# Optimization experiments

Measured on AMD Instinct MI355X. Metric: run time of the kernel, lower is better.

## Reference

```python
import jax, jax.numpy as jnp
import numpy as np

NUM_HEADS = 8
NS = 27  # 3x3x3 deformable samples per query


def _resize1d(x, axis, new):
    # linear resize along one axis, align_corners=False (matches F.interpolate); identity if size matches
    old = x.shape[axis]
    if old == new:
        return x
    pos = (jnp.arange(new, dtype=jnp.float32) + 0.5) * (old / new) - 0.5
    f = jnp.floor(pos)
    w = pos - f
    i0 = jnp.clip(f, 0, old - 1).astype(jnp.int32)
    i1 = jnp.clip(f + 1, 0, old - 1).astype(jnp.int32)
    shp = [1] * x.ndim
    shp[axis] = new
    w = w.reshape(shp)
    return jnp.take(x, i0, axis=axis) * (1 - w) + jnp.take(x, i1, axis=axis) * w


def _rel_to_abs(x):
    # x: (b, d, h, w, w+NS-1) -> (b, d, h, w, NS) via the pad/reshape shifting trick
    b, d, h, w, c = x.shape
    x = jnp.pad(x, ((0, 0), (0, 0), (0, 0), (0, 0), (0, 1)))
    x = x.reshape(b, d, h, w * (c + 1))
    x = jnp.pad(x, ((0, 0), (0, 0), (0, 0), (0, NS - 1)))
    x = x.reshape(b, d, h, w + 1, NS + w - 1)
    return x[:, :, :, :w, w - 1:]


def _rel_logits_1d(q, rel_k):
    # q: (BH, 1, A, B, C, hd); rel_k: (C+NS-1, hd) -> (BH, A, B, C, NS)
    logits = jnp.einsum('nzxywd,rd->nzxywr', q, rel_k)
    n, z, a, b, c, r = logits.shape
    return _rel_to_abs(logits.reshape(n, z * a, b, c, r))


def _pos_emb(q, rel_depth, rel_height, rel_width, D, H, W):
    # q: (BH, 1, D, H, W, hd) -> (BH, D, H, W, NS)
    rw = _resize1d(rel_width, 0, W + NS - 1)
    rh = _resize1d(rel_height, 0, H + NS - 1)
    rd = _resize1d(rel_depth, 0, D + NS - 1)
    lw = _rel_logits_1d(q, rw)            # (BH, D, H, W, NS)
    qh = jnp.swapaxes(q, 3, 4)            # (BH, 1, D, W, H, hd)
    lh = _rel_logits_1d(qh, rh)           # (BH, D, W, H, NS)
    qd = jnp.swapaxes(qh, 2, 4)           # (BH, 1, H, W, D, hd)
    ld = _rel_logits_1d(qd, rd)           # (BH, H, W, D, NS)
    # trilinear resize of lh/ld to (D, H, W) over spatial axes (identity when D==H==W)
    for ax, tgt in ((1, D), (2, H), (3, W)):
        lh = _resize1d(lh, ax, tgt)
        ld = _resize1d(ld, ax, tgt)
    return lw + lh + ld


def _deform_unfold3d(x, offset):
    # x: (BH, C, D, H, W); offset: (BH, NS*3, D, H, W) -> (BH, C*NS, D*H*W)
    BH, C, D, H, W = x.shape
    off = offset.reshape(BH, NS, 3, D, H, W)
    k = jnp.arange(NS)
    kz = (k // 9 - 1).astype(jnp.float32)
    ky = (k // 3 % 3 - 1).astype(jnp.float32)
    kx = (k % 3 - 1).astype(jnp.float32)
    zz, yy, xx = jnp.meshgrid(jnp.arange(D, dtype=jnp.float32),
                              jnp.arange(H, dtype=jnp.float32),
                              jnp.arange(W, dtype=jnp.float32), indexing='ij')
    pz = zz + kz[:, None, None, None] + off[:, :, 0]   # (BH, NS, D, H, W)
    py = yy + ky[:, None, None, None] + off[:, :, 1]
    px = xx + kx[:, None, None, None] + off[:, :, 2]
    z0 = jnp.floor(pz); y0 = jnp.floor(py); x0 = jnp.floor(px)
    wz = pz - z0; wy = py - y0; wx = px - x0
    z0 = z0.astype(jnp.int32); y0 = y0.astype(jnp.int32); x0 = x0.astype(jnp.int32)
    S = D * H * W
    xf = x.reshape(BH, C, S)
    acc = jnp.zeros((BH, C, NS * S), dtype=x.dtype)
    for dz in (0, 1):
        for dy in (0, 1):
            for dx in (0, 1):
                zi = z0 + dz; yi = y0 + dy; xi = x0 + dx
                valid = ((zi >= 0) & (zi < D) & (yi >= 0) & (yi < H) & (xi >= 0) & (xi < W)).astype(x.dtype)
                w = (wz if dz else 1 - wz) * (wy if dy else 1 - wy) * (wx if dx else 1 - wx) * valid
                idx = (jnp.clip(zi, 0, D - 1) * H + jnp.clip(yi, 0, H - 1)) * W + jnp.clip(xi, 0, W - 1)
                g = jnp.take_along_axis(xf, idx.reshape(BH, 1, NS * S), axis=2)  # (BH, C, NS*S)
                acc = acc + g * w.reshape(BH, 1, NS * S)
    return acc.reshape(BH, C * NS, S)


def _forward(x, w_qkv, w_proj, b_proj, w_off, rel_depth, rel_height, rel_width, D, H, W):
    B, N, C = x.shape
    nh = NUM_HEADS
    hd = C // nh
    scale = hd ** -0.5
    BH = B * nh
    qkv = (x @ w_qkv.T).reshape(B, N, 3, nh, hd)
    q = qkv[:, :, 0].transpose(0, 2, 1, 3)  # (B, nh, N, hd)
    k = qkv[:, :, 1].transpose(0, 2, 1, 3)
    v = qkv[:, :, 2].transpose(0, 2, 1, 3)
    offset = (x.reshape(B, N, nh, hd) @ w_off.T).transpose(0, 2, 3, 1).reshape(BH, NS * 3, D, H, W)
    kmap = k.transpose(0, 1, 3, 2).reshape(BH, hd, D, H, W)
    vmap = v.transpose(0, 1, 3, 2).reshape(BH, hd, D, H, W)
    ks = _deform_unfold3d(kmap, offset).transpose(0, 2, 1).reshape(B, nh, N, hd, NS)
    vs = _deform_unfold3d(vmap, offset).reshape(B, nh, hd, NS, N).transpose(0, 1, 4, 3, 2)  # (B, nh, N, NS, hd)
    attn = jnp.einsum('bhnd,bhnds->bhns', q, ks) * scale
    pos = _pos_emb(q.reshape(BH, 1, D, H, W, hd), rel_depth, rel_height, rel_width, D, H, W).reshape(B, nh, N, NS)
    attn = jax.nn.softmax(attn + pos, axis=-1)
    out = jnp.einsum('bhns,bhnsd->bhnd', attn, vs).transpose(0, 2, 1, 3).reshape(B, N, C)
    return out @ w_proj.T + b_proj


def setup_inputs():
    key = jax.random.key(0)
    ks = jax.random.split(key, 8)
    B, D, H, W, C = 1, 16, 16, 16, 512
    N = D * H * W
    hd = C // NUM_HEADS
    return {
        'x': jax.random.normal(ks[0], (B, N, C), dtype=jnp.float32),
        'w_qkv': jax.random.normal(ks[1], (3 * C, C), dtype=jnp.float32) * 0.02,
        'w_proj': jax.random.normal(ks[2], (C, C), dtype=jnp.float32) * 0.02,
        'b_proj': jnp.zeros((C,), dtype=jnp.float32),
        'w_off': jax.random.normal(ks[3], (NS * 3, hd), dtype=jnp.float32) * 0.01,
        'rel_depth': jax.random.normal(ks[4], (D + NS - 1, hd), dtype=jnp.float32) * hd ** -0.5,
        'rel_height': jax.random.normal(ks[5], (H + NS - 1, hd), dtype=jnp.float32) * hd ** -0.5,
        'rel_width': jax.random.normal(ks[6], (W + NS - 1, hd), dtype=jnp.float32) * hd ** -0.5,
        'D': D, 'H': H, 'W': W,
    }


def reference(x, w_qkv, w_proj, b_proj, w_off, rel_depth, rel_height, rel_width, D, H, W):
    return _forward(x, w_qkv, w_proj, b_proj, w_off, rel_depth, rel_height, rel_width, D, H, W)
```

## Files before the change

### kernel.cpp

```cpp
#include <hip/hip_runtime.h>
#include <hip/hip_fp16.h>
#include <math.h>
#include <stdint.h>

#define NH    8
#define HD    64
#define NTOK  4096
#define CDIM  512
#define NSAMP 27

typedef __attribute__((ext_vector_type(8))) _Float16 half8;
typedef __attribute__((ext_vector_type(4))) float floatx4;
typedef unsigned short ushort_t;

__device__ __forceinline__ ushort_t f16b(float f) {
  return __half_as_ushort(__float2half(f));
}
__device__ __forceinline__ __half2 u2h2(uint32_t u) { return __builtin_bit_cast(__half2, u); }
__device__ __forceinline__ uint32_t h22u(__half2 h) { return __builtin_bit_cast(uint32_t, h); }

__device__ __forceinline__ float wave_sum_lane63(float x) {
#define DPP_STEP(ctrl, rmask)                                                   \
  { int t = __builtin_amdgcn_update_dpp(0, __float_as_int(x), ctrl, rmask, 0xf, \
                                        true);                                  \
    x += __int_as_float(t); }
  DPP_STEP(0x111, 0xf)
  DPP_STEP(0x112, 0xf)
  DPP_STEP(0x114, 0xf)
  DPP_STEP(0x118, 0xf)
  DPP_STEP(0x142, 0xa)
  DPP_STEP(0x143, 0xc)
#undef DPP_STEP
  return x;
}

__global__ __launch_bounds__(256) void k_cvt(const float* __restrict__ x,
                                             const float* __restrict__ wq,
                                             const float* __restrict__ wp,
                                             const float* __restrict__ w_off,
                                             const float* __restrict__ rel_d,
                                             const float* __restrict__ rel_h,
                                             const float* __restrict__ rel_w,
                                             ushort_t* __restrict__ xb,
                                             ushort_t* __restrict__ wqb,
                                             ushort_t* __restrict__ wpb,
                                             ushort_t* __restrict__ w_offh,
                                             ushort_t* __restrict__ relh) {
  int i = blockIdx.x * 256 + threadIdx.x;
  const float4* src = nullptr;
  ushort_t* dst;
  int off;
  float4 v = make_float4(0.f, 0.f, 0.f, 0.f);
  if (i < 524288)      { src = (const float4*)x;  dst = xb;  off = i; }
  else if (i < 720896) { src = (const float4*)wq; dst = wqb; off = i - 524288; }
  else if (i < 786432) { src = (const float4*)wp; dst = wpb; off = i - 720896; }
  else {
    int t = i - 786432;
    if (t < 2048) {
      off = t;
      int e = t * 4, row = e >> 6;
      if (row < 81) v = *(const float4*)&w_off[e];
      dst = w_offh;
    } else {
      off = t - 2048;
      int e = off * 4, row = e >> 6, col = e & 63;
      if (row < 42)       v = *(const float4*)&rel_w[row * 64 + col];
      else if (row < 84)  v = *(const float4*)&rel_h[(row - 42) * 64 + col];
      else if (row < 126) v = *(const float4*)&rel_d[(row - 84) * 64 + col];
      dst = relh;
    }
  }
  if (src) v = src[off];
  ushort4 o = make_ushort4(f16b(v.x), f16b(v.y), f16b(v.z), f16b(v.w));
  *(ushort4*)&dst[(size_t)off * 4] = o;
}

__global__ __launch_bounds__(256) void k_qkv(const ushort_t* __restrict__ Ah,
                                             const ushort_t* __restrict__ Bth,
                                             ushort_t* __restrict__ qh16,
                                             uint32_t* __restrict__ kvb) {
  __shared__ __align__(16) ushort_t As[128 * 32];
  __shared__ __align__(16) ushort_t Bs[128 * 32];
  const int tid = threadIdx.x;
  const int wave = tid >> 6, lane = tid & 63;
  const int wr = wave >> 1, wc = wave & 1;
  const int m15 = lane & 15, quad = lane >> 4;
  const int bm = blockIdx.x, bn = blockIdx.y;
  floatx4 acc[4][4];
#pragma unroll
  for (int i = 0; i < 4; i++)
#pragma unroll
    for (int j = 0; j < 4; j++) acc[i][j] = {0.f, 0.f, 0.f, 0.f};

  const int r0 = tid >> 2, c0 = (tid & 3) * 8;
  const int r1 = r0 + 64;
  for (int k0 = 0; k0 < 512; k0 += 32) {
    *(uint4*)&As[r0 * 32 + c0] = *(const uint4*)&Ah[(size_t)(bm * 128 + r0) * 512 + k0 + c0];
    *(uint4*)&As[r1 * 32 + c0] = *(const uint4*)&Ah[(size_t)(bm * 128 + r1) * 512 + k0 + c0];
    *(uint4*)&Bs[r0 * 32 + c0] = *(const uint4*)&Bth[(size_t)(bn * 128 + r0) * 512 + k0 + c0];
    *(uint4*)&Bs[r1 * 32 + c0] = *(const uint4*)&Bth[(size_t)(bn * 128 + r1) * 512 + k0 + c0];
    __syncthreads();
    half8 af[4], bf[4];
#pragma unroll
    for (int i = 0; i < 4; i++)
      af[i] = *(const half8*)&As[(wr * 64 + i * 16 + m15) * 32 + quad * 8];
#pragma unroll
    for (int j = 0; j < 4; j++)
      bf[j] = *(const half8*)&Bs[(wc * 64 + j * 16 + m15) * 32 + quad * 8];
#pragma unroll
    for (int i = 0; i < 4; i++)
#pragma unroll
      for (int j = 0; j < 4; j++)
        acc[i][j] = __builtin_amdgcn_mfma_f32_16x16x32_f16(af[i], bf[j], acc[i][j], 0, 0, 0);
    __syncthreads();
  }

  ushort_t* kvh16 = (ushort_t*)kvb;
#pragma unroll
  for (int i = 0; i < 4; i++)
#pragma unroll
    for (int j = 0; j < 4; j++) {
      int col = bn * 128 + wc * 64 + j * 16 + m15;
      int t = col >> 9;
      int h = (col >> 6) & 7;
      int d = col & 63;
#pragma unroll
      for (int r = 0; r < 4; r++) {
        int row = bm * 128 + wr * 64 + i * 16 + quad * 4 + r;
        size_t idx = ((size_t)h * NTOK + row) * 64 + d;
        float v = acc[i][j][r];
        if (t == 0) qh16[idx] = f16b(v);
        else kvh16[idx * 2 + (t - 1)] = f16b(v);
      }
    }
}

__global__ __launch_bounds__(256) void k_aux(const ushort_t* __restrict__ xh,
                                             const ushort_t* __restrict__ qh16,
                                             const ushort_t* __restrict__ w_offh,
                                             const ushort_t* __restrict__ relh,
                                             float* __restrict__ ob,
                                             float* __restrict__ Pb) {
  __shared__ __align__(16) ushort_t As[128 * 32];
  __shared__ __align__(16) ushort_t Bs[128 * 32];
  const int tid = threadIdx.x;
  const int wave = tid >> 6, lane = tid & 63;
  const int wr = wave >> 1, wc = wave & 1;
  const int m15 = lane & 15, quad = lane >> 4;
  const int bm = blockIdx.x;
  const int mode = blockIdx.y >> 3, h = blockIdx.y & 7;

  const ushort_t* A;  int lda;
  const ushort_t* B;
  float* C;  int NC;
  if (mode == 0) { A = xh + h * 64;                  lda = 512; B = w_offh; C = ob + (size_t)h * NTOK * 81;  NC = 81; }
  else           { A = qh16 + (size_t)h * NTOK * 64; lda = 64;  B = relh;   C = Pb + (size_t)h * NTOK * 126; NC = 126; }

  floatx4 acc[4][4];
#pragma unroll
  for (int i = 0; i < 4; i++)
#pragma unroll
    for (int j = 0; j < 4; j++) acc[i][j] = {0.f, 0.f, 0.f, 0.f};

  const int r0 = tid >> 2, c0 = (tid & 3) * 8;
  const int r1 = r0 + 64;
  for (int k0 = 0; k0 < 64; k0 += 32) {
    *(uint4*)&As[r0 * 32 + c0] = *(const uint4*)&A[(size_t)(bm * 128 + r0) * lda + k0 + c0];
    *(uint4*)&As[r1 * 32 + c0] = *(const uint4*)&A[(size_t)(bm * 128 + r1) * lda + k0 + c0];
    *(uint4*)&Bs[r0 * 32 + c0] = *(const uint4*)&B[(size_t)r0 * 64 + k0 + c0];
    *(uint4*)&Bs[r1 * 32 + c0] = *(const uint4*)&B[(size_t)r1 * 64 + k0 + c0];
    __syncthreads();
    half8 af[4], bf[4];
#pragma unroll
    for (int i = 0; i < 4; i++)
      af[i] = *(const half8*)&As[(wr * 64 + i * 16 + m15) * 32 + quad * 8];
#pragma unroll
    for (int j = 0; j < 4; j++)
      bf[j] = *(const half8*)&Bs[(wc * 64 + j * 16 + m15) * 32 + quad * 8];
#pragma unroll
    for (int i = 0; i < 4; i++)
#pragma unroll
      for (int j = 0; j < 4; j++)
        acc[i][j] = __builtin_amdgcn_mfma_f32_16x16x32_f16(af[i], bf[j], acc[i][j], 0, 0, 0);
    __syncthreads();
  }

#pragma unroll
  for (int i = 0; i < 4; i++)
#pragma unroll
    for (int j = 0; j < 4; j++) {
      int col = wc * 64 + j * 16 + m15;
      if (col < NC) {
#pragma unroll
        for (int r = 0; r < 4; r++) {
          int row = bm * 128 + wr * 64 + i * 16 + quad * 4 + r;
          C[(size_t)row * NC + col] = acc[i][j][r];
        }
      }
    }
}

__global__ __launch_bounds__(256) void k_attn(const ushort_t* __restrict__ qh16,
                                              const uint32_t* __restrict__ kvb,
                                              const float* __restrict__ obuf,
                                              const float* __restrict__ Pbuf,
                                              ushort_t* __restrict__ attb16) {
  __shared__ int      s_off[4][NSAMP][8];
  __shared__ uint32_t s_cwh[4][NSAMP][8];
  __shared__ uint32_t vpair[4][14][64];
  __shared__ float    s_dots[4][NSAMP];
  __shared__ uint32_t s_wp[4][14];
  const int bid = blockIdx.x;
  const int h = bid & 7;
  const int wave = threadIdx.x >> 6;
  const int lane = threadIdx.x & 63;
  const int n = (bid >> 3) * 4 + wave;
  const int z = n >> 8, y = (n >> 4) & 15, xq = n & 15;
  const float qd = __half2float(__ushort_as_half(qh16[((size_t)h * NTOK + n) * 64 + lane]));
  const char* kvc = (const char*)(kvb + (size_t)h * NTOK * 64);
  const uint32_t lane4 = (uint32_t)lane * 4u;

  if (lane < 54) {
    const int s = lane >> 1, half = lane & 1;
    const float* op = &obuf[((size_t)h * NTOK + n) * 81 + s * 3];
    float oz = op[0], oy = op[1], ox = op[2];
    float pz = (float)(z + (s / 9) - 1) + oz;
    float py = (float)(y + ((s / 3) % 3) - 1) + oy;
    float px = (float)(xq + (s % 3) - 1) + ox;
    float fz = floorf(pz), fy = floorf(py), fx = floorf(px);
    float wz = pz - fz, wy = py - fy, wx = px - fx;
    int z0 = (int)fz, y0 = (int)fy, x0 = (int)fx;
    int      oarr[4];
    uint32_t warr[4];
#pragma unroll
    for (int cc = 0; cc < 4; cc++) {
      int c = half * 4 + cc;
      int dz = (c >> 2) & 1, dy = (c >> 1) & 1, dx = c & 1;
      int zi = z0 + dz, yi = y0 + dy, xi = x0 + dx;
      bool valid = (zi >= 0) && (zi < 16) && (yi >= 0) && (yi < 16) && (xi >= 0) && (xi < 16);
      float w = (dz ? wz : 1.f - wz) * (dy ? wy : 1.f - wy) * (dx ? wx : 1.f - wx);
      int zc = min(max(zi, 0), 15), yc = min(max(yi, 0), 15), xc = min(max(xi, 0), 15);
      oarr[cc] = ((zc * 16 + yc) * 16 + xc) * 256;
      uint32_t hw = (uint32_t)f16b(valid ? w : 0.f);
      warr[cc] = hw | (hw << 16);
    }
    *(int4*)&s_off[wave][s][half * 4]  = make_int4(oarr[0], oarr[1], oarr[2], oarr[3]);
    *(uint4*)&s_cwh[wave][s][half * 4] = make_uint4(warr[0], warr[1], warr[2], warr[3]);
  }

  const bool writer = (lane == 63);
  uint32_t prev_acc = 0;
#pragma unroll
  for (int s = 0; s < NSAMP; s++) {
    int4  o0 = *(const int4*)&s_off[wave][s][0];
    int4  o1 = *(const int4*)&s_off[wave][s][4];
    uint4 c0 = *(const uint4*)&s_cwh[wave][s][0];
    uint4 c1 = *(const uint4*)&s_cwh[wave][s][4];
    __half2 acc2 = u2h2(0u);
    uint32_t p;
#define CORNER(OV, WV)                                                       \
    p = *(const uint32_t*)(kvc + (uint32_t)((uint32_t)OV + lane4));          \
    acc2 = __hfma2(u2h2(WV), u2h2(p), acc2);
    CORNER(o0.x, c0.x) CORNER(o0.y, c0.y) CORNER(o0.z, c0.z) CORNER(o0.w, c0.w)
    CORNER(o1.x, c1.x) CORNER(o1.y, c1.y) CORNER(o1.z, c1.z) CORNER(o1.w, c1.w)
#undef CORNER
    float ak = __half2float(acc2.x);
    float tot = wave_sum_lane63(qd * ak);
    if (writer) s_dots[wave][s] = tot;
    uint32_t au = h22u(acc2);
    if (s & 1)
      vpair[wave][s >> 1][lane] = (prev_acc >> 16) | (au & 0xffff0000u);
    else
      prev_acc = au;
  }
  vpair[wave][13][lane] = prev_acc >> 16;

  float logit = -INFINITY;
  if (lane < NSAMP) {
    int j = 15 + lane - xq;
    int n2 = (z * 16 + xq) * 16 + y;
    int n3 = (xq * 16 + z) * 16 + y;
    float pos = Pbuf[((size_t)h * NTOK + n) * 126 + j]
              + Pbuf[((size_t)h * NTOK + n2) * 126 + 42 + j]
              + Pbuf[((size_t)h * NTOK + n3) * 126 + 84 + j];
    logit = s_dots[wave][lane] * 0.125f + pos;
  }

  float mx = logit;
#pragma unroll
  for (int off = 32; off >= 1; off >>= 1) mx = fmaxf(mx, __shfl_xor(mx, off, 64));
  float e = __expf(logit - mx);
  float sum = e;
#pragma unroll
  for (int off = 32; off >= 1; off >>= 1) sum += __shfl_xor(sum, off, 64);
  const float wgt = e / sum;
  uint32_t hw = (uint32_t)f16b(wgt);
  uint32_t nw = (uint32_t)__shfl_down((int)hw, 1, 64);
  if ((lane & 1) == 0 && lane < 28)
    s_wp[wave][lane >> 1] = hw | (nw << 16);

  __half2 out2 = u2h2(0u);
#pragma unroll
  for (int p2 = 0; p2 < 14; p2++) {
    __half2 v2 = u2h2(vpair[wave][p2][lane]);
    out2 = __hfma2(u2h2(s_wp[wave][p2]), v2, out2);
  }
  float out = __half2float(out2.x) + __half2float(out2.y);
  attb16[(size_t)n * 512 + h * 64 + lane] = f16b(out);
}

__global__ __launch_bounds__(256) void k_proj(const ushort_t* __restrict__ Ah,
                                              const ushort_t* __restrict__ Bth,
                                              const float* __restrict__ bias,
                                              float* __restrict__ out) {
  __shared__ __align__(16) ushort_t As[128 * 32];
  __shared__ __align__(16) ushort_t Bs[128 * 32];
  const int tid = threadIdx.x;
  const int wave = tid >> 6, lane = tid & 63;
  const int wr = wave >> 1, wc = wave & 1;
  const int m15 = lane & 15, quad = lane >> 4;
  const int bm = blockIdx.x, bn = blockIdx.y;
  floatx4 acc[4][4];
#pragma unroll
  for (int i = 0; i < 4; i++)
#pragma unroll
    for (int j = 0; j < 4; j++) acc[i][j] = {0.f, 0.f, 0.f, 0.f};

  const int r0 = tid >> 2, c0 = (tid & 3) * 8;
  const int r1 = r0 + 64;
  for (int k0 = 0; k0 < 512; k0 += 32) {
    *(uint4*)&As[r0 * 32 + c0] = *(const uint4*)&Ah[(size_t)(bm * 128 + r0) * 512 + k0 + c0];
    *(uint4*)&As[r1 * 32 + c0] = *(const uint4*)&Ah[(size_t)(bm * 128 + r1) * 512 + k0 + c0];
    *(uint4*)&Bs[r0 * 32 + c0] = *(const uint4*)&Bth[(size_t)(bn * 128 + r0) * 512 + k0 + c0];
    *(uint4*)&Bs[r1 * 32 + c0] = *(const uint4*)&Bth[(size_t)(bn * 128 + r1) * 512 + k0 + c0];
    __syncthreads();
    half8 af[4], bf[4];
#pragma unroll
    for (int i = 0; i < 4; i++)
      af[i] = *(const half8*)&As[(wr * 64 + i * 16 + m15) * 32 + quad * 8];
#pragma unroll
    for (int j = 0; j < 4; j++)
      bf[j] = *(const half8*)&Bs[(wc * 64 + j * 16 + m15) * 32 + quad * 8];
#pragma unroll
    for (int i = 0; i < 4; i++)
#pragma unroll
      for (int j = 0; j < 4; j++)
        acc[i][j] = __builtin_amdgcn_mfma_f32_16x16x32_f16(af[i], bf[j], acc[i][j], 0, 0, 0);
    __syncthreads();
  }

#pragma unroll
  for (int i = 0; i < 4; i++)
#pragma unroll
    for (int j = 0; j < 4; j++) {
      int col = bn * 128 + wc * 64 + j * 16 + m15;
      float b = bias[col];
#pragma unroll
      for (int r = 0; r < 4; r++) {
        int row = bm * 128 + wr * 64 + i * 16 + quad * 4 + r;
        out[(size_t)row * 512 + col] = acc[i][j][r] + b;
      }
    }
}

extern "C" void kernel_launch(void* const* d_in, const int* in_sizes, int n_in,
                              void* d_out, int out_size, void* d_ws, size_t ws_size,
                              hipStream_t stream) {
  const float* x      = (const float*)d_in[0];
  const float* w_qkv  = (const float*)d_in[1];
  const float* w_proj = (const float*)d_in[2];
  const float* b_proj = (const float*)d_in[3];
  const float* w_off  = (const float*)d_in[4];
  const float* rel_d  = (const float*)d_in[5];
  const float* rel_h  = (const float*)d_in[6];
  const float* rel_w  = (const float*)d_in[7];

  char* ws = (char*)d_ws;
  uint32_t* kvb    = (uint32_t*)ws; ws += (size_t)NH * NTOK * 64 * 4;
  float*    ob     = (float*)ws;    ws += (size_t)NH * NTOK * 81 * 4;
  float*    Pb     = (float*)ws;    ws += (size_t)NH * NTOK * 126 * 4;
  ushort_t* attb16 = (ushort_t*)ws; ws += (size_t)NTOK * CDIM * 2;
  ushort_t* xh     = (ushort_t*)ws; ws += (size_t)NTOK * CDIM * 2;
  ushort_t* wqh    = (ushort_t*)ws; ws += (size_t)3 * CDIM * CDIM * 2;
  ushort_t* wph    = (ushort_t*)ws; ws += (size_t)CDIM * CDIM * 2;
  ushort_t* qh16   = (ushort_t*)ws; ws += (size_t)NH * NTOK * 64 * 2;
  ushort_t* w_offh = (ushort_t*)ws; ws += (size_t)128 * 64 * 2;
  ushort_t* relh   = (ushort_t*)ws; ws += (size_t)128 * 64 * 2;
  float*    out    = (float*)d_out;

  k_cvt <<<dim3(3088), dim3(256), 0, stream>>>(x, w_qkv, w_proj, w_off, rel_d, rel_h,
                                               rel_w, xh, wqh, wph, w_offh, relh);
  k_qkv <<<dim3(32, 12), dim3(256), 0, stream>>>(xh, wqh, qh16, kvb);
  k_aux <<<dim3(32, 16), dim3(256), 0, stream>>>(xh, qh16, w_offh, relh, ob, Pb);
  k_attn<<<dim3(8192),   dim3(256), 0, stream>>>(qh16, kvb, ob, Pb, attb16);
  k_proj<<<dim3(32, 4),  dim3(256), 0, stream>>>(attb16, wph, b_proj, out);
}
```

Before: 189.8 us.

## Stage QKV epilogue through LDS and broadcast attention dots via readlane

The QKV GEMM now groups each head's K and V weight rows into a single output block. Its epilogue goes through shared memory, so q and the interleaved k/v pairs are written as coalesced 16-byte stores instead of scattered 2-byte stores. In the attention kernel, each of the first 27 lanes computes all 8 trilinear corners for one sample. Per-sample dot products are broadcast with readlane and kept in a register, which removes the s_dots shared array, and the sample loop is only partially unrolled. The extra ~35KB LDS staging buffer in the GEMM may reduce occupancy.

```diff
diff --git a/kernel.cpp b/kernel.cpp
--- a/kernel.cpp
+++ b/kernel.cpp
@@ -19,7 +19,7 @@
 __device__ __forceinline__ __half2 u2h2(uint32_t u) { return __builtin_bit_cast(__half2, u); }
 __device__ __forceinline__ uint32_t h22u(__half2 h) { return __builtin_bit_cast(uint32_t, h); }
 
-__device__ __forceinline__ float wave_sum_lane63(float x) {
+__device__ __forceinline__ float wave_sum_bcast(float x) {
 #define DPP_STEP(ctrl, rmask)                                                   \
   { int t = __builtin_amdgcn_update_dpp(0, __float_as_int(x), ctrl, rmask, 0xf, \
                                         true);                                  \
@@ -31,7 +31,7 @@
   DPP_STEP(0x142, 0xa)
   DPP_STEP(0x143, 0xc)
 #undef DPP_STEP
-  return x;
+  return __int_as_float(__builtin_amdgcn_readlane(__float_as_int(x), 63));
 }
 
 __global__ __launch_bounds__(256) void k_cvt(const float* __restrict__ x,
@@ -81,11 +81,14 @@
                                              uint32_t* __restrict__ kvb) {
   __shared__ __align__(16) ushort_t As[128 * 32];
   __shared__ __align__(16) ushort_t Bs[128 * 32];
+  __shared__ __align__(16) ushort_t Cs[128 * 136];
   const int tid = threadIdx.x;
   const int wave = tid >> 6, lane = tid & 63;
   const int wr = wave >> 1, wc = wave & 1;
   const int m15 = lane & 15, quad = lane >> 4;
   const int bm = blockIdx.x, bn = blockIdx.y;
+  const bool is_q = (bn < 4);
+  const int h = bn - 4;
   floatx4 acc[4][4];
 #pragma unroll
   for (int i = 0; i < 4; i++)
@@ -94,11 +97,13 @@
 
   const int r0 = tid >> 2, c0 = (tid & 3) * 8;
   const int r1 = r0 + 64;
+  const int brA = is_q ? (bn * 128 + r0) : (512 + h * 64 + r0);
+  const int brB = is_q ? (bn * 128 + r1) : (1024 + h * 64 + r0);
   for (int k0 = 0; k0 < 512; k0 += 32) {
     *(uint4*)&As[r0 * 32 + c0] = *(const uint4*)&Ah[(size_t)(bm * 128 + r0) * 512 + k0 + c0];
     *(uint4*)&As[r1 * 32 + c0] = *(const uint4*)&Ah[(size_t)(bm * 128 + r1) * 512 + k0 + c0];
-    *(uint4*)&Bs[r0 * 32 + c0] = *(const uint4*)&Bth[(size_t)(bn * 128 + r0) * 512 + k0 + c0];
-    *(uint4*)&Bs[r1 * 32 + c0] = *(const uint4*)&Bth[(size_t)(bn * 128 + r1) * 512 + k0 + c0];
+    *(uint4*)&Bs[r0 * 32 + c0] = *(const uint4*)&Bth[(size_t)brA * 512 + k0 + c0];
+    *(uint4*)&Bs[r1 * 32 + c0] = *(const uint4*)&Bth[(size_t)brB * 512 + k0 + c0];
     __syncthreads();
     half8 af[4], bf[4];
 #pragma unroll
@@ -115,24 +120,43 @@
     __syncthreads();
   }
 
-  ushort_t* kvh16 = (ushort_t*)kvb;
 #pragma unroll
   for (int i = 0; i < 4; i++)
 #pragma unroll
     for (int j = 0; j < 4; j++) {
-      int col = bn * 128 + wc * 64 + j * 16 + m15;
-      int t = col >> 9;
-      int h = (col >> 6) & 7;
-      int d = col & 63;
+      int col = wc * 64 + j * 16 + m15;
 #pragma unroll
       for (int r = 0; r < 4; r++) {
-        int row = bm * 128 + wr * 64 + i * 16 + quad * 4 + r;
-        size_t idx = ((size_t)h * NTOK + row) * 64 + d;
-        float v = acc[i][j][r];
-        if (t == 0) qh16[idx] = f16b(v);
-        else kvh16[idx * 2 + (t - 1)] = f16b(v);
+        int row = wr * 64 + i * 16 + quad * 4 + r;
+        Cs[row * 136 + col] = f16b(acc[i][j][r]);
       }
     }
+  __syncthreads();
+
+  if (is_q) {
+#pragma unroll
+    for (int it = 0; it < 8; it++) {
+      int id = it * 256 + tid;
+      int hh = id >> 10, row = (id >> 3) & 127, chunk = id & 7;
+      uint4 d = *(const uint4*)&Cs[row * 136 + hh * 64 + chunk * 8];
+      int hq = bn * 2 + hh;
+      *(uint4*)&qh16[((size_t)hq * NTOK + bm * 128 + row) * 64 + chunk * 8] = d;
+    }
+  } else {
+#pragma unroll
+    for (int it = 0; it < 8; it++) {
+      int id = it * 256 + tid;
+      int row = id >> 4, chunk = id & 15;
+      uint2 kk = *(const uint2*)&Cs[row * 136 + chunk * 4];
+      uint2 vv = *(const uint2*)&Cs[row * 136 + 64 + chunk * 4];
+      uint4 o;
+      o.x = (kk.x & 0xffffu) | (vv.x << 16);
+      o.y = (kk.x >> 16) | (vv.x & 0xffff0000u);
+      o.z = (kk.y & 0xffffu) | (vv.y << 16);
+      o.w = (kk.y >> 16) | (vv.y & 0xffff0000u);
+      *(uint4*)&kvb[((size_t)h * NTOK + bm * 128 + row) * 64 + chunk * 4] = o;
+    }
+  }
 }
 
 __global__ __launch_bounds__(256) void k_aux(const ushort_t* __restrict__ xh,
@@ -208,7 +232,6 @@
   __shared__ int      s_off[4][NSAMP][8];
   __shared__ uint32_t s_cwh[4][NSAMP][8];
   __shared__ uint32_t vpair[4][14][64];
-  __shared__ float    s_dots[4][NSAMP];
   __shared__ uint32_t s_wp[4][14];
   const int bid = blockIdx.x;
   const int h = bid & 7;
@@ -220,8 +243,8 @@
   const char* kvc = (const char*)(kvb + (size_t)h * NTOK * 64);
   const uint32_t lane4 = (uint32_t)lane * 4u;
 
-  if (lane < 54) {
-    const int s = lane >> 1, half = lane & 1;
+  if (lane < NSAMP) {
+    const int s = lane;
     const float* op = &obuf[((size_t)h * NTOK + n) * 81 + s * 3];
     float oz = op[0], oy = op[1], ox = op[2];
     float pz = (float)(z + (s / 9) - 1) + oz;
@@ -230,27 +253,28 @@
     float fz = floorf(pz), fy = floorf(py), fx = floorf(px);
     float wz = pz - fz, wy = py - fy, wx = px - fx;
     int z0 = (int)fz, y0 = (int)fy, x0 = (int)fx;
-    int      oarr[4];
-    uint32_t warr[4];
-#pragma unroll
-    for (int cc = 0; cc < 4; cc++) {
-      int c = half * 4 + cc;
+    int      oarr[8];
+    uint32_t warr[8];
+#pragma unroll
+    for (int c = 0; c < 8; c++) {
       int dz = (c >> 2) & 1, dy = (c >> 1) & 1, dx = c & 1;
       int zi = z0 + dz, yi = y0 + dy, xi = x0 + dx;
       bool valid = (zi >= 0) && (zi < 16) && (yi >= 0) && (yi < 16) && (xi >= 0) && (xi < 16);
       float w = (dz ? wz : 1.f - wz) * (dy ? wy : 1.f - wy) * (dx ? wx : 1.f - wx);
       int zc = min(max(zi, 0), 15), yc = min(max(yi, 0), 15), xc = min(max(xi, 0), 15);
-      oarr[cc] = ((zc * 16 + yc) * 16 + xc) * 256;
+      oarr[c] = ((zc * 16 + yc) * 16 + xc) * 256;
       uint32_t hw = (uint32_t)f16b(valid ? w : 0.f);
-      warr[cc] = hw | (hw << 16);
-    }
-    *(int4*)&s_off[wave][s][half * 4]  = make_int4(oarr[0], oarr[1], oarr[2], oarr[3]);
-    *(uint4*)&s_cwh[wave][s][half * 4] = make_uint4(warr[0], warr[1], warr[2], warr[3]);
-  }
-
-  const bool writer = (lane == 63);
+      warr[c] = hw | (hw << 16);
+    }
+    *(int4*)&s_off[wave][s][0]  = make_int4(oarr[0], oarr[1], oarr[2], oarr[3]);
+    *(int4*)&s_off[wave][s][4]  = make_int4(oarr[4], oarr[5], oarr[6], oarr[7]);
+    *(uint4*)&s_cwh[wave][s][0] = make_uint4(warr[0], warr[1], warr[2], warr[3]);
+    *(uint4*)&s_cwh[wave][s][4] = make_uint4(warr[4], warr[5], warr[6], warr[7]);
+  }
+
+  float mydot = 0.f;
   uint32_t prev_acc = 0;
-#pragma unroll
+#pragma unroll 2
   for (int s = 0; s < NSAMP; s++) {
     int4  o0 = *(const int4*)&s_off[wave][s][0];
     int4  o1 = *(const int4*)&s_off[wave][s][4];
@@ -265,8 +289,8 @@
     CORNER(o1.x, c1.x) CORNER(o1.y, c1.y) CORNER(o1.z, c1.z) CORNER(o1.w, c1.w)
 #undef CORNER
     float ak = __half2float(acc2.x);
-    float tot = wave_sum_lane63(qd * ak);
-    if (writer) s_dots[wave][s] = tot;
+    float tot = wave_sum_bcast(qd * ak);
+    mydot = (lane == s) ? tot : mydot;
     uint32_t au = h22u(acc2);
     if (s & 1)
       vpair[wave][s >> 1][lane] = (prev_acc >> 16) | (au & 0xffff0000u);
@@ -283,7 +307,7 @@
     float pos = Pbuf[((size_t)h * NTOK + n) * 126 + j]
               + Pbuf[((size_t)h * NTOK + n2) * 126 + 42 + j]
               + Pbuf[((size_t)h * NTOK + n3) * 126 + 84 + j];
-    logit = s_dots[wave][lane] * 0.125f + pos;
+    logit = mydot * 0.125f + pos;
   }
 
   float mx = logit;
@@ -303,7 +327,8 @@
 #pragma unroll
   for (int p2 = 0; p2 < 14; p2++) {
     __half2 v2 = u2h2(vpair[wave][p2][lane]);
-    out2 = __hfma2(u2h2(s_wp[wave][p2]), v2, out2);
+    __half2 w2 = u2h2(s_wp[wave][p2]);
+    out2 = __hfma2(w2, v2, out2);
   }
   float out = __half2float(out2.x) + __half2float(out2.y);
   attb16[(size_t)n * 512 + h * 64 + lane] = f16b(out);
```

New measurement: 181.6 us. -4.4%, faster.
